# Kernel tuning notes

Hardware: AMD Instinct MI355X
Metric: run time of the kernel (lower is better)

The kernel has to match this reference:

```python
import jax, jax.numpy as jnp
import numpy as np

D_K = 24
ALPHA = 0.1
N_HEADS = 6
D_MODEL = 144
LN_EPS = 1e-5


def setup_inputs() -> dict:
    key = jax.random.key(0)
    ks = jax.random.split(key, 8)
    B, S = 8, 2048
    Q = jax.random.normal(ks[0], (B, S, D_MODEL), dtype=jnp.float32)
    K = jax.random.normal(ks[1], (B, N_HEADS, S, D_K), dtype=jnp.float32)
    V = jax.random.normal(ks[2], (B, N_HEADS, S, D_K), dtype=jnp.float32)
    attn_mask = jax.random.randint(ks[3], (B, S, S), 0, 2).astype(bool)
    Wq_w = jax.random.normal(ks[4], (D_MODEL, D_MODEL), dtype=jnp.float32) * 0.05
    Wq_b = jnp.zeros((D_MODEL,), dtype=jnp.float32)
    lin_w = jax.random.normal(ks[5], (D_MODEL, D_MODEL), dtype=jnp.float32) * 0.05
    lin_b = jnp.zeros((D_MODEL,), dtype=jnp.float32)
    ln_g = jnp.ones((D_MODEL,), dtype=jnp.float32)
    ln_b = jnp.zeros((D_MODEL,), dtype=jnp.float32)
    return {"Q": Q, "K": K, "V": V, "attn_mask": attn_mask,
            "Wq_w": Wq_w, "Wq_b": Wq_b, "lin_w": lin_w, "lin_b": lin_b,
            "ln_g": ln_g, "ln_b": ln_b}


def reference(Q, K, V, attn_mask, Wq_w, Wq_b, lin_w, lin_b, ln_g, ln_b):
    B, S, _ = Q.shape
    residual = Q
    # W_Q projection then head split: [B,S,D] -> [B,H,S,d_k]
    q = (Q @ Wq_w.T + Wq_b).reshape(B, S, N_HEADS, D_K).transpose(0, 2, 1, 3)
    # scores [B,H,S,Sk]; custom tanh activation instead of softmax
    scores = jnp.einsum('bhqd,bhkd->bhqk', q, K) / np.sqrt(D_K).astype(np.float32)
    attn = jnp.tanh(ALPHA * scores)
    # NOTE: original calls attn.masked_fill(...) non-inplace and drops the
    # result, so attn_mask has no effect. Faithfully ignored here.
    context = jnp.einsum('bhqk,bhkd->bhqd', attn, V)
    context = context.transpose(0, 2, 1, 3).reshape(B, S, N_HEADS * D_K)
    output = context @ lin_w.T + lin_b
    x = output + residual
    mu = jnp.mean(x, axis=-1, keepdims=True)
    var = jnp.var(x, axis=-1, keepdims=True)
    return (x - mu) / jnp.sqrt(var + LN_EPS) * ln_g + ln_b
```

## Files before the change

kernel.cpp:

```cpp
#include <hip/hip_runtime.h>
#include <hip/hip_bf16.h>

#define B_  8
#define S_  2048
#define H_  6
#define DK_ 24
#define DM_ 144
#define SCALE_ 0.020412414523193153f

typedef __bf16 bf16x8 __attribute__((ext_vector_type(8)));
typedef __bf16 bf16x2 __attribute__((ext_vector_type(2)));
typedef float  f32x4  __attribute__((ext_vector_type(4)));

__device__ __forceinline__ unsigned short f2bf(float f) {
    return __builtin_bit_cast(unsigned short, (__bf16)f);
}
__device__ __forceinline__ uint pack2(float a, float b) {
    bf16x2 v; v[0] = (__bf16)a; v[1] = (__bf16)b;
    return __builtin_bit_cast(uint, v);
}
__device__ __forceinline__ float tanh7(float x) {
    float t = x * x;
    float u = fmaf(t, -5.3968254e-02f, 1.3333333e-01f);
    u = fmaf(t, u, -3.3333333e-01f);
    u = fmaf(t, u, 1.0f);
    return x * u;
}

__global__ __launch_bounds__(256)
void prep_w_kernel(const float* __restrict__ Wq, const float* __restrict__ Wqb,
                   const float* __restrict__ Wl, const float* __restrict__ lb,
                   ushort* __restrict__ Whq, ushort* __restrict__ Wlp) {
    int i = blockIdx.x * 256 + threadIdx.x;
    if (i < 30720) {
        int h = i / 5120, rem = i % 5120;
        int d = rem / 160, c = rem % 160;
        float v = 0.f;
        if (d < DK_) {
            if (c < DM_)       v = Wq[(h * DK_ + d) * DM_ + c];
            else if (c == DM_) v = Wqb[h * DK_ + d];
        }
        Whq[i] = f2bf(v);
    } else if (i < 53760) {
        int j = i - 30720;
        int r = j / 160, c = j % 160;
        float v = (c < DM_) ? Wl[r * DM_ + c] : (c == DM_ ? lb[r] : 0.f);
        Wlp[j] = f2bf(v);
    }
}

__global__ __launch_bounds__(256)
void prep_v_kernel(const float* __restrict__ V, ushort* __restrict__ Vtt) {
    __shared__ float sv[64 * 25];
    const int t = threadIdx.x;
    const int kt = blockIdx.x, h = blockIdx.y, b = blockIdx.z;
    const int bh = b * H_ + h;
    const float4* Vs = (const float4*)(V + ((size_t)bh * S_ + kt * 64) * DK_);
    for (int idx = t; idx < 384; idx += 256) {
        int r = idx / 6, c4 = (idx % 6) * 4;
        *(float4*)&sv[r * 25 + c4] = Vs[idx];
    }
    __syncthreads();
    int d = t >> 3, s8 = (t & 7) * 8;
    uint4 o = {0u, 0u, 0u, 0u};
    if (d < DK_) {
        o.x = pack2(sv[(s8 + 0) * 25 + d], sv[(s8 + 1) * 25 + d]);
        o.y = pack2(sv[(s8 + 2) * 25 + d], sv[(s8 + 3) * 25 + d]);
        o.z = pack2(sv[(s8 + 4) * 25 + d], sv[(s8 + 5) * 25 + d]);
        o.w = pack2(sv[(s8 + 6) * 25 + d], sv[(s8 + 7) * 25 + d]);
    }
    ((uint4*)Vtt)[((size_t)(bh * 32 + kt) * 32 + d) * 8 + (t & 7)] = o;
}

__global__ __launch_bounds__(256)
void attn_kernel(const float* __restrict__ Q, const ushort* __restrict__ Whq,
                 const float* __restrict__ Kg, const ushort* __restrict__ Vtt,
                 float* __restrict__ out) {
    __shared__ __attribute__((aligned(16))) char smem[37376];
    ushort* s_q  = (ushort*)smem;
    ushort* s_a  = (ushort*)(smem + 5120);
    ushort* s_w  = (ushort*)(smem + 26624);
    ushort* s_k  = (ushort*)(smem + 5120);
    ushort* s_vt = (ushort*)(smem + 15360);
    ushort* s_p  = (ushort*)(smem + 24576);
    float*  s_ctx= (float*)(smem + 24576);

    const int t = threadIdx.x;
    const int w = t >> 6, lane = t & 63, n16 = lane & 15, g = lane >> 4;
    const int qt = blockIdx.x, h = blockIdx.y, b = blockIdx.z;
    const int bh = b * H_ + h;

    const float4* Qs = (const float4*)(Q + ((size_t)b * S_ + qt * 64) * DM_);
    for (int idx = t; idx < 2304; idx += 256) {
        int r = idx / 36, c4 = (idx % 36) * 4;
        float4 v = Qs[idx];
        uint2 u; u.x = pack2(v.x, v.y); u.y = pack2(v.z, v.w);
        *(uint2*)&s_a[r * 168 + c4] = u;
    }
    if (t < 64) {
        uint4 pad = {0x00003F80u, 0u, 0u, 0u};
        uint4 z4  = {0u, 0u, 0u, 0u};
        *(uint4*)&s_a[t * 168 + 144] = pad;
        *(uint4*)&s_a[t * 168 + 152] = z4;
    }
    const uint4* Ws = (const uint4*)(Whq + h * 5120);
    for (int idx = t; idx < 640; idx += 256) {
        int r = idx / 20, c8 = (idx % 20) * 8;
        *(uint4*)&s_w[r * 168 + c8] = Ws[idx];
    }
    __syncthreads();

    const f32x4 zf = {0.f, 0.f, 0.f, 0.f};
    f32x4 qacc0 = zf, qacc1 = zf;
#pragma unroll
    for (int ks = 0; ks < 5; ++ks) {
        bf16x8 av = *(const bf16x8*)&s_a[(w * 16 + n16) * 168 + ks * 32 + g * 8];
        bf16x8 b0 = *(const bf16x8*)&s_w[n16 * 168 + ks * 32 + g * 8];
        bf16x8 b1 = *(const bf16x8*)&s_w[(16 + n16) * 168 + ks * 32 + g * 8];
        qacc0 = __builtin_amdgcn_mfma_f32_16x16x32_bf16(av, b0, qacc0, 0, 0, 0);
        qacc1 = __builtin_amdgcn_mfma_f32_16x16x32_bf16(av, b1, qacc1, 0, 0, 0);
    }
#pragma unroll
    for (int reg = 0; reg < 4; ++reg) {
        int r = (w * 16 + g * 4 + reg) * 40;
        s_q[r + n16]      = f2bf(qacc0[reg]);
        s_q[r + 16 + n16] = f2bf(qacc1[reg]);
    }
    __syncthreads();

    for (int idx = t; idx < 512; idx += 256) {
        int buf = idx >> 8, r = (idx >> 2) & 63, c2 = idx & 3;
        *(uint*)&s_k[buf * 2560 + r * 40 + 24 + 2 * c2] = 0u;
    }
    const bf16x8 qf = *(const bf16x8*)&s_q[(w * 16 + n16) * 40 + g * 8];

    const float4*  Kbase = (const float4*)(Kg + (size_t)bh * S_ * DK_);
    const uint4*   Vbase = (const uint4*)Vtt + (size_t)(bh * 32) * 256;
    const int r1 = t / 6,          c1 = (t % 6) * 4;
    const int r2 = (t + 256) / 6,  c2 = ((t + 256) % 6) * 4;
    const int vt_off = (t >> 3) * 72 + (t & 7) * 8;

    float4 ka, kb2; uint4 vv;
    ka = Kbase[t];
    if (t < 128) kb2 = Kbase[t + 256];
    vv = Vbase[t];

    f32x4 acc0 = zf, acc1 = zf;
    int p = 0;
    for (int kt = 0; kt < 32; ++kt) {
        {
            uint2 u; u.x = pack2(ka.x, ka.y); u.y = pack2(ka.z, ka.w);
            *(uint2*)&s_k[p * 2560 + r1 * 40 + c1] = u;
            if (t < 128) {
                uint2 u2; u2.x = pack2(kb2.x, kb2.y); u2.y = pack2(kb2.z, kb2.w);
                *(uint2*)&s_k[p * 2560 + r2 * 40 + c2] = u2;
            }
            *(uint4*)&s_vt[p * 2304 + vt_off] = vv;
        }
        __syncthreads();
        if (kt < 31) {
            const float4* Kn = Kbase + (kt + 1) * 384;
            ka = Kn[t];
            if (t < 128) kb2 = Kn[t + 256];
            vv = Vbase[(kt + 1) * 256 + t];
        }
#pragma unroll
        for (int mt = 0; mt < 4; ++mt) {
            bf16x8 a = *(const bf16x8*)&s_k[p * 2560 + (mt * 16 + n16) * 40 + g * 8];
            f32x4 c = __builtin_amdgcn_mfma_f32_16x16x32_bf16(a, qf, zf, 0, 0, 0);
            uint2 u;
            u.x = pack2(tanh7(SCALE_ * c[0]), tanh7(SCALE_ * c[1]));
            u.y = pack2(tanh7(SCALE_ * c[2]), tanh7(SCALE_ * c[3]));
            *(uint2*)&s_p[(w * 16 + n16) * 72 + mt * 16 + g * 4] = u;
        }
#pragma unroll
        for (int ks = 0; ks < 2; ++ks) {
            bf16x8 ap = *(const bf16x8*)&s_p[(w * 16 + n16) * 72 + ks * 32 + g * 8];
            bf16x8 b0 = *(const bf16x8*)&s_vt[p * 2304 + n16 * 72 + ks * 32 + g * 8];
            bf16x8 b1 = *(const bf16x8*)&s_vt[p * 2304 + (16 + n16) * 72 + ks * 32 + g * 8];
            acc0 = __builtin_amdgcn_mfma_f32_16x16x32_bf16(ap, b0, acc0, 0, 0, 0);
            acc1 = __builtin_amdgcn_mfma_f32_16x16x32_bf16(ap, b1, acc1, 0, 0, 0);
        }
        p ^= 1;
    }

    __syncthreads();
#pragma unroll
    for (int reg = 0; reg < 4; ++reg) {
        int row = w * 16 + g * 4 + reg;
        s_ctx[row * 28 + n16] = acc0[reg];
        if (n16 < 8) s_ctx[row * 28 + 16 + n16] = acc1[reg];
    }
    __syncthreads();
    for (int idx = t; idx < 384; idx += 256) {
        int r = idx / 6, c = idx % 6;
        float4 v4 = *(const float4*)&s_ctx[r * 28 + c * 4];
        *(float4*)&out[((size_t)b * S_ + qt * 64 + r) * DM_ + h * DK_ + c * 4] = v4;
    }
}

__global__ __launch_bounds__(512)
void outln_kernel(const float* __restrict__ Qres, const ushort* __restrict__ Wlp,
                  const float* __restrict__ lg, const float* __restrict__ lbeta,
                  float* __restrict__ io) {
    __shared__ __attribute__((aligned(16))) ushort s_a[64 * 168];
    __shared__ __attribute__((aligned(16))) ushort s_w[144 * 168];
    __shared__ float s_red[2][2][64];
    const int t = threadIdx.x;
    const int w = t >> 6, lane = t & 63, n16 = lane & 15, g = lane >> 4;
    const int wq = w & 3, half = w >> 2;
    const int nt_base = half * 5, nt_cnt = half ? 4 : 5;
    const int row0 = blockIdx.x * 64;

    for (int idx = t; idx < 2304; idx += 512) {
        int r = idx / 36, c4 = (idx % 36) * 4;
        float4 v = *(const float4*)&io[(size_t)(row0 + r) * DM_ + c4];
        uint2 u; u.x = pack2(v.x, v.y); u.y = pack2(v.z, v.w);
        *(uint2*)&s_a[r * 168 + c4] = u;
    }
    if (t < 64) {
        uint4 pad = {0x00003F80u, 0u, 0u, 0u};
        uint4 z4  = {0u, 0u, 0u, 0u};
        *(uint4*)&s_a[t * 168 + 144] = pad;
        *(uint4*)&s_a[t * 168 + 152] = z4;
    }
    for (int idx = t; idx < 2880; idx += 512) {
        int r = idx / 20, c8 = (idx % 20) * 8;
        *(uint4*)&s_w[r * 168 + c8] = *(const uint4*)&Wlp[r * 160 + c8];
    }
    __syncthreads();

    f32x4 acc[5];
#pragma unroll
    for (int j = 0; j < 5; ++j) acc[j] = (f32x4){0.f, 0.f, 0.f, 0.f};
#pragma unroll
    for (int ks = 0; ks < 5; ++ks) {
        bf16x8 av = *(const bf16x8*)&s_a[(wq * 16 + n16) * 168 + ks * 32 + g * 8];
        for (int j = 0; j < nt_cnt; ++j) {
            bf16x8 bv = *(const bf16x8*)&s_w[((nt_base + j) * 16 + n16) * 168 + ks * 32 + g * 8];
            acc[j] = __builtin_amdgcn_mfma_f32_16x16x32_bf16(av, bv, acc[j], 0, 0, 0);
        }
    }
    float vals[5][4], s1[4] = {0, 0, 0, 0}, s2[4] = {0, 0, 0, 0};
    for (int j = 0; j < nt_cnt; ++j) {
        int d = (nt_base + j) * 16 + n16;
#pragma unroll
        for (int reg = 0; reg < 4; ++reg) {
            int row = row0 + wq * 16 + g * 4 + reg;
            float v = acc[j][reg] + Qres[(size_t)row * DM_ + d];
            vals[j][reg] = v;
            s1[reg] += v; s2[reg] = fmaf(v, v, s2[reg]);
        }
    }
#pragma unroll
    for (int off = 1; off < 16; off <<= 1) {
#pragma unroll
        for (int reg = 0; reg < 4; ++reg) {
            s1[reg] += __shfl_xor(s1[reg], off);
            s2[reg] += __shfl_xor(s2[reg], off);
        }
    }
    if (n16 == 0) {
#pragma unroll
        for (int reg = 0; reg < 4; ++reg) {
            int rr = wq * 16 + g * 4 + reg;
            s_red[half][0][rr] = s1[reg];
            s_red[half][1][rr] = s2[reg];
        }
    }
    __syncthreads();
    float mu[4], rs[4];
#pragma unroll
    for (int reg = 0; reg < 4; ++reg) {
        int rr = wq * 16 + g * 4 + reg;
        float S1 = s_red[0][0][rr] + s_red[1][0][rr];
        float S2 = s_red[0][1][rr] + s_red[1][1][rr];
        float m = S1 * (1.f / 144.f);
        mu[reg] = m;
        rs[reg] = rsqrtf(S2 * (1.f / 144.f) - m * m + 1e-5f);
    }
    for (int j = 0; j < nt_cnt; ++j) {
        int d = (nt_base + j) * 16 + n16;
        float gv = lg[d], bv = lbeta[d];
#pragma unroll
        for (int reg = 0; reg < 4; ++reg) {
            int row = row0 + wq * 16 + g * 4 + reg;
            io[(size_t)row * DM_ + d] = (vals[j][reg] - mu[reg]) * rs[reg] * gv + bv;
        }
    }
}

extern "C" void kernel_launch(void* const* d_in, const int* in_sizes, int n_in,
                              void* d_out, int out_size, void* d_ws, size_t ws_size,
                              hipStream_t stream) {
    const float* Q     = (const float*)d_in[0];
    const float* K     = (const float*)d_in[1];
    const float* V     = (const float*)d_in[2];
    const float* Wq_w  = (const float*)d_in[4];
    const float* Wq_b  = (const float*)d_in[5];
    const float* lin_w = (const float*)d_in[6];
    const float* lin_b = (const float*)d_in[7];
    const float* ln_g  = (const float*)d_in[8];
    const float* ln_b  = (const float*)d_in[9];
    float* out = (float*)d_out;

    ushort* Vtt = (ushort*)d_ws;
    ushort* Whq = (ushort*)((char*)d_ws + 6291456);
    ushort* Wlp = (ushort*)((char*)d_ws + 6291456 + 61440);

    prep_w_kernel<<<210, 256, 0, stream>>>(Wq_w, Wq_b, lin_w, lin_b, Whq, Wlp);
    prep_v_kernel<<<dim3(32, H_, B_), 256, 0, stream>>>(V, Vtt);
    attn_kernel<<<dim3(S_ / 64, H_, B_), 256, 0, stream>>>(Q, Whq, K, Vtt, out);
    outln_kernel<<<(B_ * S_) / 64, 512, 0, stream>>>(Q, Wlp, ln_g, ln_b, out);
}
```

Measured before the change: 274.1 us.

## Process 128 query rows per block, pre-convert K to bf16, fold scale into tanh

The attention kernel now handles 128 query rows per block in two 64-row sub-tiles that share each staged K/V tile, which halves K/V global and LDS traffic per query row. K is converted to padded bf16 in the prep kernel alongside V, so the main loop only copies uint4 values instead of converting fp32. The tanh polynomial coefficients absorb the score scale and alpha, removing a multiply per element. The trade-offs are half as many blocks (768) competing for occupancy, a larger LDS footprint, and an extra K write/read pass in the prep kernel.

```diff
diff --git a/kernel.cpp b/kernel.cpp
--- a/kernel.cpp
+++ b/kernel.cpp
@@ -6,7 +6,11 @@
 #define H_  6
 #define DK_ 24
 #define DM_ 144
-#define SCALE_ 0.020412414523193153f
+
+#define TK0  2.0412414523193153e-02f
+#define TK1 -2.8350575726379381e-06f
+#define TK2  4.7250959543965635e-10f
+#define TK3 -7.9686705934386491e-14f
 
 typedef __bf16 bf16x8 __attribute__((ext_vector_type(8)));
 typedef __bf16 bf16x2 __attribute__((ext_vector_type(2)));
@@ -19,12 +23,12 @@
     bf16x2 v; v[0] = (__bf16)a; v[1] = (__bf16)b;
     return __builtin_bit_cast(uint, v);
 }
-__device__ __forceinline__ float tanh7(float x) {
-    float t = x * x;
-    float u = fmaf(t, -5.3968254e-02f, 1.3333333e-01f);
-    u = fmaf(t, u, -3.3333333e-01f);
-    u = fmaf(t, u, 1.0f);
-    return x * u;
+__device__ __forceinline__ float tanh_s(float c) {
+    float t = c * c;
+    float u = fmaf(t, TK3, TK2);
+    u = fmaf(t, u, TK1);
+    u = fmaf(t, u, TK0);
+    return c * u;
 }
 
 __global__ __launch_bounds__(256)
@@ -50,11 +54,22 @@
 }
 
 __global__ __launch_bounds__(256)
-void prep_v_kernel(const float* __restrict__ V, ushort* __restrict__ Vtt) {
+void prep_kv_kernel(const float* __restrict__ K, const float* __restrict__ V,
+                    ushort* __restrict__ Ktt, ushort* __restrict__ Vtt) {
     __shared__ float sv[64 * 25];
     const int t = threadIdx.x;
     const int kt = blockIdx.x, h = blockIdx.y, b = blockIdx.z;
     const int bh = b * H_ + h;
+    const size_t tile = (size_t)(bh * 32 + kt);
+    const float4* Ks = (const float4*)(K + ((size_t)bh * S_ + kt * 64) * DK_);
+    ushort* Ko = Ktt + tile * 2048;
+    for (int idx = t; idx < 384; idx += 256) {
+        int r = idx / 6, c4 = (idx % 6) * 4;
+        float4 v = Ks[idx];
+        ushort4 u; u.x = f2bf(v.x); u.y = f2bf(v.y); u.z = f2bf(v.z); u.w = f2bf(v.w);
+        *(ushort4*)&Ko[r * 32 + c4] = u;
+    }
+    if (t < 64) { uint4 z = {0u,0u,0u,0u}; *(uint4*)&Ko[t * 32 + 24] = z; }
     const float4* Vs = (const float4*)(V + ((size_t)bh * S_ + kt * 64) * DK_);
     for (int idx = t; idx < 384; idx += 256) {
         int r = idx / 6, c4 = (idx % 6) * 4;
@@ -62,124 +77,154 @@
     }
     __syncthreads();
     int d = t >> 3, s8 = (t & 7) * 8;
-    uint4 o = {0u, 0u, 0u, 0u};
+    uint4 o = {0u,0u,0u,0u};
     if (d < DK_) {
         o.x = pack2(sv[(s8 + 0) * 25 + d], sv[(s8 + 1) * 25 + d]);
         o.y = pack2(sv[(s8 + 2) * 25 + d], sv[(s8 + 3) * 25 + d]);
         o.z = pack2(sv[(s8 + 4) * 25 + d], sv[(s8 + 5) * 25 + d]);
         o.w = pack2(sv[(s8 + 6) * 25 + d], sv[(s8 + 7) * 25 + d]);
     }
-    ((uint4*)Vtt)[((size_t)(bh * 32 + kt) * 32 + d) * 8 + (t & 7)] = o;
+    ((uint4*)Vtt)[tile * 256 + t] = o;
 }
 
 __global__ __launch_bounds__(256)
 void attn_kernel(const float* __restrict__ Q, const ushort* __restrict__ Whq,
-                 const float* __restrict__ Kg, const ushort* __restrict__ Vtt,
+                 const ushort* __restrict__ Ktt, const ushort* __restrict__ Vtt,
                  float* __restrict__ out) {
-    __shared__ __attribute__((aligned(16))) char smem[37376];
+    __shared__ __attribute__((aligned(16))) char smem[42496];
     ushort* s_q  = (ushort*)smem;
-    ushort* s_a  = (ushort*)(smem + 5120);
-    ushort* s_w  = (ushort*)(smem + 26624);
-    ushort* s_k  = (ushort*)(smem + 5120);
-    ushort* s_vt = (ushort*)(smem + 15360);
-    ushort* s_p  = (ushort*)(smem + 24576);
-    float*  s_ctx= (float*)(smem + 24576);
+    ushort* s_k  = (ushort*)(smem + 10240);
+    ushort* s_vt = (ushort*)(smem + 20480);
+    ushort* s_p  = (ushort*)(smem + 29696);
+    ushort* s_a  = (ushort*)(smem + 10240);
+    ushort* s_w  = (ushort*)(smem + 31744);
+    float*  s_ctx= (float*)(smem + 10240);
 
     const int t = threadIdx.x;
-    const int w = t >> 6, lane = t & 63, n16 = lane & 15, g = lane >> 4;
-    const int qt = blockIdx.x, h = blockIdx.y, b = blockIdx.z;
+    const int w = t >> 6, n16 = t & 15, g = (t >> 4) & 3;
+    const int qp = blockIdx.x, h = blockIdx.y, b = blockIdx.z;
     const int bh = b * H_ + h;
-
-    const float4* Qs = (const float4*)(Q + ((size_t)b * S_ + qt * 64) * DM_);
-    for (int idx = t; idx < 2304; idx += 256) {
-        int r = idx / 36, c4 = (idx % 36) * 4;
-        float4 v = Qs[idx];
-        uint2 u; u.x = pack2(v.x, v.y); u.y = pack2(v.z, v.w);
-        *(uint2*)&s_a[r * 168 + c4] = u;
-    }
-    if (t < 64) {
-        uint4 pad = {0x00003F80u, 0u, 0u, 0u};
-        uint4 z4  = {0u, 0u, 0u, 0u};
-        *(uint4*)&s_a[t * 168 + 144] = pad;
-        *(uint4*)&s_a[t * 168 + 152] = z4;
-    }
+    const int row0 = qp * 128;
+
+    const uint4* Kb = (const uint4*)(Ktt + (size_t)bh * 65536);
+    const uint4* Vb = (const uint4*)(Vtt + (size_t)bh * 65536);
+    uint4 kv = Kb[t], vv = Vb[t];
+
     const uint4* Ws = (const uint4*)(Whq + h * 5120);
     for (int idx = t; idx < 640; idx += 256) {
         int r = idx / 20, c8 = (idx % 20) * 8;
         *(uint4*)&s_w[r * 168 + c8] = Ws[idx];
     }
-    __syncthreads();
-
     const f32x4 zf = {0.f, 0.f, 0.f, 0.f};
-    f32x4 qacc0 = zf, qacc1 = zf;
-#pragma unroll
-    for (int ks = 0; ks < 5; ++ks) {
-        bf16x8 av = *(const bf16x8*)&s_a[(w * 16 + n16) * 168 + ks * 32 + g * 8];
-        bf16x8 b0 = *(const bf16x8*)&s_w[n16 * 168 + ks * 32 + g * 8];
-        bf16x8 b1 = *(const bf16x8*)&s_w[(16 + n16) * 168 + ks * 32 + g * 8];
-        qacc0 = __builtin_amdgcn_mfma_f32_16x16x32_bf16(av, b0, qacc0, 0, 0, 0);
-        qacc1 = __builtin_amdgcn_mfma_f32_16x16x32_bf16(av, b1, qacc1, 0, 0, 0);
-    }
-#pragma unroll
-    for (int reg = 0; reg < 4; ++reg) {
-        int r = (w * 16 + g * 4 + reg) * 40;
-        s_q[r + n16]      = f2bf(qacc0[reg]);
-        s_q[r + 16 + n16] = f2bf(qacc1[reg]);
-    }
-    __syncthreads();
-
-    for (int idx = t; idx < 512; idx += 256) {
-        int buf = idx >> 8, r = (idx >> 2) & 63, c2 = idx & 3;
-        *(uint*)&s_k[buf * 2560 + r * 40 + 24 + 2 * c2] = 0u;
-    }
-    const bf16x8 qf = *(const bf16x8*)&s_q[(w * 16 + n16) * 40 + g * 8];
-
-    const float4*  Kbase = (const float4*)(Kg + (size_t)bh * S_ * DK_);
-    const uint4*   Vbase = (const uint4*)Vtt + (size_t)(bh * 32) * 256;
-    const int r1 = t / 6,          c1 = (t % 6) * 4;
-    const int r2 = (t + 256) / 6,  c2 = ((t + 256) % 6) * 4;
-    const int vt_off = (t >> 3) * 72 + (t & 7) * 8;
-
-    float4 ka, kb2; uint4 vv;
-    ka = Kbase[t];
-    if (t < 128) kb2 = Kbase[t + 256];
-    vv = Vbase[t];
-
-    f32x4 acc0 = zf, acc1 = zf;
+#pragma unroll
+    for (int pass = 0; pass < 2; ++pass) {
+        const float4* Qs = (const float4*)(Q + ((size_t)b * S_ + row0 + pass * 64) * DM_);
+        for (int idx = t; idx < 2304; idx += 256) {
+            int r = idx / 36, c4 = (idx % 36) * 4;
+            float4 v = Qs[idx];
+            uint2 u; u.x = pack2(v.x, v.y); u.y = pack2(v.z, v.w);
+            *(uint2*)&s_a[r * 168 + c4] = u;
+        }
+        if (t < 64) {
+            uint4 pad = {0x00003F80u, 0u, 0u, 0u};
+            uint4 z4  = {0u, 0u, 0u, 0u};
+            *(uint4*)&s_a[t * 168 + 144] = pad;
+            *(uint4*)&s_a[t * 168 + 152] = z4;
+        }
+        __syncthreads();
+        f32x4 qa0 = zf, qa1 = zf;
+#pragma unroll
+        for (int ks = 0; ks < 5; ++ks) {
+            bf16x8 av = *(const bf16x8*)&s_a[(w * 16 + n16) * 168 + ks * 32 + g * 8];
+            bf16x8 b0 = *(const bf16x8*)&s_w[n16 * 168 + ks * 32 + g * 8];
+            bf16x8 b1 = *(const bf16x8*)&s_w[(16 + n16) * 168 + ks * 32 + g * 8];
+            qa0 = __builtin_amdgcn_mfma_f32_16x16x32_bf16(av, b0, qa0, 0, 0, 0);
+            qa1 = __builtin_amdgcn_mfma_f32_16x16x32_bf16(av, b1, qa1, 0, 0, 0);
+        }
+#pragma unroll
+        for (int reg = 0; reg < 4; ++reg) {
+            int r = (pass * 64 + w * 16 + g * 4 + reg) * 40;
+            s_q[r + n16]      = f2bf(qa0[reg]);
+            s_q[r + 16 + n16] = f2bf(qa1[reg]);
+        }
+        __syncthreads();
+    }
+
+    const bf16x8 qf0 = *(const bf16x8*)&s_q[(w * 16 + n16) * 40 + g * 8];
+    const bf16x8 qf1 = *(const bf16x8*)&s_q[(64 + w * 16 + n16) * 40 + g * 8];
+
+    const int koff = (t >> 2) * 40 + (t & 3) * 8;
+    const int voff = (t >> 3) * 72 + (t & 7) * 8;
+    const int prow = (w * 16 + n16) * 72;
+
+    f32x4 acc00 = zf, acc01 = zf, acc10 = zf, acc11 = zf;
     int p = 0;
     for (int kt = 0; kt < 32; ++kt) {
+        *(uint4*)&s_k[p * 2560 + koff] = kv;
+        *(uint4*)&s_vt[p * 2304 + voff] = vv;
+        __syncthreads();
         {
-            uint2 u; u.x = pack2(ka.x, ka.y); u.y = pack2(ka.z, ka.w);
-            *(uint2*)&s_k[p * 2560 + r1 * 40 + c1] = u;
-            if (t < 128) {
-                uint2 u2; u2.x = pack2(kb2.x, kb2.y); u2.y = pack2(kb2.z, kb2.w);
-                *(uint2*)&s_k[p * 2560 + r2 * 40 + c2] = u2;
-            }
-            *(uint4*)&s_vt[p * 2304 + vt_off] = vv;
-        }
-        __syncthreads();
-        if (kt < 31) {
-            const float4* Kn = Kbase + (kt + 1) * 384;
-            ka = Kn[t];
-            if (t < 128) kb2 = Kn[t + 256];
-            vv = Vbase[(kt + 1) * 256 + t];
-        }
-#pragma unroll
-        for (int mt = 0; mt < 4; ++mt) {
-            bf16x8 a = *(const bf16x8*)&s_k[p * 2560 + (mt * 16 + n16) * 40 + g * 8];
-            f32x4 c = __builtin_amdgcn_mfma_f32_16x16x32_bf16(a, qf, zf, 0, 0, 0);
+            int nt = (kt + 1) & 31;
+            kv = Kb[nt * 256 + t];
+            vv = Vb[nt * 256 + t];
+        }
+        bf16x8 a0 = *(const bf16x8*)&s_k[p * 2560 + n16 * 40 + g * 8];
+        bf16x8 a1 = *(const bf16x8*)&s_k[p * 2560 + (16 + n16) * 40 + g * 8];
+        bf16x8 a2 = *(const bf16x8*)&s_k[p * 2560 + (32 + n16) * 40 + g * 8];
+        bf16x8 a3 = *(const bf16x8*)&s_k[p * 2560 + (48 + n16) * 40 + g * 8];
+        bf16x8 vb00 = *(const bf16x8*)&s_vt[p * 2304 + n16 * 72 + g * 8];
+        bf16x8 vb01 = *(const bf16x8*)&s_vt[p * 2304 + (16 + n16) * 72 + g * 8];
+        bf16x8 vb10 = *(const bf16x8*)&s_vt[p * 2304 + n16 * 72 + 32 + g * 8];
+        bf16x8 vb11 = *(const bf16x8*)&s_vt[p * 2304 + (16 + n16) * 72 + 32 + g * 8];
+        {
+            f32x4 c0 = __builtin_amdgcn_mfma_f32_16x16x32_bf16(a0, qf0, zf, 0, 0, 0);
+            f32x4 c1 = __builtin_amdgcn_mfma_f32_16x16x32_bf16(a1, qf0, zf, 0, 0, 0);
+            f32x4 c2 = __builtin_amdgcn_mfma_f32_16x16x32_bf16(a2, qf0, zf, 0, 0, 0);
+            f32x4 c3 = __builtin_amdgcn_mfma_f32_16x16x32_bf16(a3, qf0, zf, 0, 0, 0);
             uint2 u;
-            u.x = pack2(tanh7(SCALE_ * c[0]), tanh7(SCALE_ * c[1]));
-            u.y = pack2(tanh7(SCALE_ * c[2]), tanh7(SCALE_ * c[3]));
-            *(uint2*)&s_p[(w * 16 + n16) * 72 + mt * 16 + g * 4] = u;
-        }
-#pragma unroll
-        for (int ks = 0; ks < 2; ++ks) {
-            bf16x8 ap = *(const bf16x8*)&s_p[(w * 16 + n16) * 72 + ks * 32 + g * 8];
-            bf16x8 b0 = *(const bf16x8*)&s_vt[p * 2304 + n16 * 72 + ks * 32 + g * 8];
-            bf16x8 b1 = *(const bf16x8*)&s_vt[p * 2304 + (16 + n16) * 72 + ks * 32 + g * 8];
-            acc0 = __builtin_amdgcn_mfma_f32_16x16x32_bf16(ap, b0, acc0, 0, 0, 0);
-            acc1 = __builtin_amdgcn_mfma_f32_16x16x32_bf16(ap, b1, acc1, 0, 0, 0);
+            u.x = pack2(tanh_s(c0[0]), tanh_s(c0[1]));
+            u.y = pack2(tanh_s(c0[2]), tanh_s(c0[3]));
+            *(uint2*)&s_p[prow + 0  + g * 4] = u;
+            u.x = pack2(tanh_s(c1[0]), tanh_s(c1[1]));
+            u.y = pack2(tanh_s(c1[2]), tanh_s(c1[3]));
+            *(uint2*)&s_p[prow + 16 + g * 4] = u;
+            u.x = pack2(tanh_s(c2[0]), tanh_s(c2[1]));
+            u.y = pack2(tanh_s(c2[2]), tanh_s(c2[3]));
+            *(uint2*)&s_p[prow + 32 + g * 4] = u;
+            u.x = pack2(tanh_s(c3[0]), tanh_s(c3[1]));
+            u.y = pack2(tanh_s(c3[2]), tanh_s(c3[3]));
+            *(uint2*)&s_p[prow + 48 + g * 4] = u;
+            bf16x8 ap0 = *(const bf16x8*)&s_p[prow + g * 8];
+            acc00 = __builtin_amdgcn_mfma_f32_16x16x32_bf16(ap0, vb00, acc00, 0, 0, 0);
+            acc01 = __builtin_amdgcn_mfma_f32_16x16x32_bf16(ap0, vb01, acc01, 0, 0, 0);
+            bf16x8 ap1 = *(const bf16x8*)&s_p[prow + 32 + g * 8];
+            acc00 = __builtin_amdgcn_mfma_f32_16x16x32_bf16(ap1, vb10, acc00, 0, 0, 0);
+            acc01 = __builtin_amdgcn_mfma_f32_16x16x32_bf16(ap1, vb11, acc01, 0, 0, 0);
+        }
+        {
+            f32x4 c0 = __builtin_amdgcn_mfma_f32_16x16x32_bf16(a0, qf1, zf, 0, 0, 0);
+            f32x4 c1 = __builtin_amdgcn_mfma_f32_16x16x32_bf16(a1, qf1, zf, 0, 0, 0);
+            f32x4 c2 = __builtin_amdgcn_mfma_f32_16x16x32_bf16(a2, qf1, zf, 0, 0, 0);
+            f32x4 c3 = __builtin_amdgcn_mfma_f32_16x16x32_bf16(a3, qf1, zf, 0, 0, 0);
+            uint2 u;
+            u.x = pack2(tanh_s(c0[0]), tanh_s(c0[1]));
+            u.y = pack2(tanh_s(c0[2]), tanh_s(c0[3]));
+            *(uint2*)&s_p[prow + 0  + g * 4] = u;
+            u.x = pack2(tanh_s(c1[0]), tanh_s(c1[1]));
+            u.y = pack2(tanh_s(c1[2]), tanh_s(c1[3]));
+            *(uint2*)&s_p[prow + 16 + g * 4] = u;
+            u.x = pack2(tanh_s(c2[0]), tanh_s(c2[1]));
+            u.y = pack2(tanh_s(c2[2]), tanh_s(c2[3]));
+            *(uint2*)&s_p[prow + 32 + g * 4] = u;
+            u.x = pack2(tanh_s(c3[0]), tanh_s(c3[1]));
+            u.y = pack2(tanh_s(c3[2]), tanh_s(c3[3]));
+            *(uint2*)&s_p[prow + 48 + g * 4] = u;
+            bf16x8 ap0 = *(const bf16x8*)&s_p[prow + g * 8];
+            acc10 = __builtin_amdgcn_mfma_f32_16x16x32_bf16(ap0, vb00, acc10, 0, 0, 0);
+            acc11 = __builtin_amdgcn_mfma_f32_16x16x32_bf16(ap0, vb01, acc11, 0, 0, 0);
+            bf16x8 ap1 = *(const bf16x8*)&s_p[prow + 32 + g * 8];
+            acc10 = __builtin_amdgcn_mfma_f32_16x16x32_bf16(ap1, vb10, acc10, 0, 0, 0);
+            acc11 = __builtin_amdgcn_mfma_f32_16x16x32_bf16(ap1, vb11, acc11, 0, 0, 0);
         }
         p ^= 1;
     }
@@ -188,14 +233,16 @@
 #pragma unroll
     for (int reg = 0; reg < 4; ++reg) {
         int row = w * 16 + g * 4 + reg;
-        s_ctx[row * 28 + n16] = acc0[reg];
-        if (n16 < 8) s_ctx[row * 28 + 16 + n16] = acc1[reg];
-    }
-    __syncthreads();
-    for (int idx = t; idx < 384; idx += 256) {
+        s_ctx[row * 28 + n16] = acc00[reg];
+        if (n16 < 8) s_ctx[row * 28 + 16 + n16] = acc01[reg];
+        s_ctx[(64 + row) * 28 + n16] = acc10[reg];
+        if (n16 < 8) s_ctx[(64 + row) * 28 + 16 + n16] = acc11[reg];
+    }
+    __syncthreads();
+    for (int idx = t; idx < 768; idx += 256) {
         int r = idx / 6, c = idx % 6;
         float4 v4 = *(const float4*)&s_ctx[r * 28 + c * 4];
-        *(float4*)&out[((size_t)b * S_ + qt * 64 + r) * DM_ + h * DK_ + c * 4] = v4;
+        *(float4*)&out[((size_t)b * S_ + row0 + r) * DM_ + h * DK_ + c * 4] = v4;
     }
 }
 
@@ -207,7 +254,7 @@
     __shared__ __attribute__((aligned(16))) ushort s_w[144 * 168];
     __shared__ float s_red[2][2][64];
     const int t = threadIdx.x;
-    const int w = t >> 6, lane = t & 63, n16 = lane & 15, g = lane >> 4;
+    const int w = t >> 6, n16 = t & 15, g = (t >> 4) & 3;
     const int wq = w & 3, half = w >> 2;
     const int nt_base = half * 5, nt_cnt = half ? 4 : 5;
     const int row0 = blockIdx.x * 64;
@@ -304,12 +351,13 @@
     const float* ln_b  = (const float*)d_in[9];
     float* out = (float*)d_out;
 
-    ushort* Vtt = (ushort*)d_ws;
-    ushort* Whq = (ushort*)((char*)d_ws + 6291456);
-    ushort* Wlp = (ushort*)((char*)d_ws + 6291456 + 61440);
+    ushort* Ktt = (ushort*)d_ws;
+    ushort* Vtt = (ushort*)((char*)d_ws + 6291456);
+    ushort* Whq = (ushort*)((char*)d_ws + 12582912);
+    ushort* Wlp = (ushort*)((char*)d_ws + 12644352);
 
     prep_w_kernel<<<210, 256, 0, stream>>>(Wq_w, Wq_b, lin_w, lin_b, Whq, Wlp);
-    prep_v_kernel<<<dim3(32, H_, B_), 256, 0, stream>>>(V, Vtt);
-    attn_kernel<<<dim3(S_ / 64, H_, B_), 256, 0, stream>>>(Q, Whq, K, Vtt, out);
+    prep_kv_kernel<<<dim3(32, H_, B_), 256, 0, stream>>>(K, V, Ktt, Vtt);
+    attn_kernel<<<dim3(S_ / 128, H_, B_), 256, 0, stream>>>(Q, Whq, Ktt, Vtt, out);
     outln_kernel<<<(B_ * S_) / 64, 512, 0, stream>>>(Q, Wlp, ln_g, ln_b, out);
 }
```

Measured after the change: 270.0 us. No clear change (-1.5%).
